# Kernel optimization log

Hardware: AMD Instinct MI355X
Metric: run time of the kernel (lower is better)

## Reference

```python
import jax, jax.numpy as jnp
import numpy as np

EMB = 64
HEADS = 8
B = 4
T = 2048


def setup_inputs() -> dict:
    key = jax.random.key(0)
    ks = jax.random.split(key, 7)
    s = 0.05
    x = jax.random.normal(ks[0], (B, T, EMB), dtype=jnp.float32)
    y = jax.random.normal(ks[1], (B, T, EMB), dtype=jnp.float32)
    mask = jax.random.randint(ks[2], (1, T, T), 0, 2, dtype=jnp.int32)
    Wk = jax.random.normal(ks[3], (EMB, EMB * HEADS), dtype=jnp.float32) * s
    Wq = jax.random.normal(ks[4], (EMB, EMB * HEADS), dtype=jnp.float32) * s
    Wv = jax.random.normal(ks[5], (EMB, EMB * HEADS), dtype=jnp.float32) * s
    Wu = jax.random.normal(ks[6], (EMB * HEADS, EMB), dtype=jnp.float32) * s
    bu = jnp.zeros((EMB,), dtype=jnp.float32)
    return {"x": x, "y": y, "mask": mask, "Wk": Wk, "Wq": Wq, "Wv": Wv, "Wu": Wu, "bu": bu}


def reference(x, y, mask, Wk, Wq, Wv, Wu, bu):
    b, t_x, e = x.shape
    _, t_y, _ = y.shape
    h = HEADS
    # projections: each head gets full dim e (head_dim == emb in this module)
    k = (x @ Wk).reshape(b, t_x, h, e).transpose(0, 2, 1, 3)  # [b,h,t_x,e]
    q = (y @ Wq).reshape(b, t_y, h, e).transpose(0, 2, 1, 3)  # [b,h,t_y,e]
    v = (x @ Wv).reshape(b, t_x, h, e).transpose(0, 2, 1, 3)  # [b,h,t_x,e]
    scale = jnp.asarray(e, x.dtype) ** 0.25
    q = q / scale
    k = k / scale
    dot = jnp.einsum('bhqe,bhke->bhqk', q, k)  # [b,h,t_y,t_x]
    # mask: [1,t_y,t_x] broadcast over batch*heads; fill -1e9 where mask==0
    dot = jnp.where(mask[:, None, :, :] == 0, jnp.asarray(-1e9, dot.dtype), dot)
    att = jax.nn.softmax(dot, axis=-1)
    out = jnp.einsum('bhqk,bhke->bqhe', att, v).reshape(b, t_y, h * e)
    return out @ Wu + bu
```

## Files before the change

### kernel.cpp

```cpp
#include <hip/hip_runtime.h>

#define EMB 64
#define HEADS 8
#define SEQ 2048
#define LSF 68

typedef short short8 __attribute__((ext_vector_type(8)));
typedef float f32x4 __attribute__((ext_vector_type(4)));
typedef unsigned int u32;

__device__ __forceinline__ float4 ld4(const float* p) { return *(const float4*)p; }
__device__ __forceinline__ float4 fmad4(float4 a, float s, float4 c) {
  c.x += a.x*s; c.y += a.y*s; c.z += a.z*s; c.w += a.w*s; return c;
}
__device__ __forceinline__ unsigned short f2bf(float f) {
  union { float f; unsigned u; } x; x.f = f;
  return (unsigned short)((x.u + 0x7fffu + ((x.u >> 16) & 1u)) >> 16);
}
__device__ __forceinline__ float bf2f(unsigned short s) {
  union { unsigned u; float f; } x; x.u = ((unsigned)s) << 16;
  return x.f;
}
__device__ __forceinline__ float bits2f(u32 u) {
  union { u32 u; float f; } x; x.u = u;
  return x.f;
}
__device__ __forceinline__ u32 cvtpk(float lo, float hi) {
  u32 r;
  asm("v_cvt_pk_bf16_f32 %0, %1, %2" : "=v"(r) : "v"(lo), "v"(hi));
  return r;
}
__device__ __forceinline__ float vexp2(float x) {
  float r;
  asm("v_exp_f32 %0, %1" : "=v"(r) : "v"(x));
  return r;
}
__device__ __forceinline__ void gload16(const void* g, void* l) {
  __builtin_amdgcn_global_load_lds((const __attribute__((address_space(1))) unsigned int*)g,
                                   (__attribute__((address_space(3))) unsigned int*)l, 16, 0, 0);
}

#define LOG2E 1.4426950408889634f
#define NC0  (-5.770780163555854f)

__global__ __launch_bounds__(256) void prep_kernel(
    const float* __restrict__ x, const float* __restrict__ y,
    const float* __restrict__ Wk, const float* __restrict__ Wq, const float* __restrict__ Wv,
    const int* __restrict__ mask, const float* __restrict__ Wu,
    unsigned short* __restrict__ Kbuf, unsigned short* __restrict__ Qbuf,
    unsigned short* __restrict__ VbufT, u32* __restrict__ pmask,
    unsigned short* __restrict__ WuThi, unsigned short* __restrict__ WuTlo)
{
  __shared__ float As[64][LSF];
  __shared__ float Bs[64][LSF];
  const int t = threadIdx.x;
  const int z = blockIdx.z;

  if (z == 3) {
    const int bid = blockIdx.x * 8 + blockIdx.y;
    #pragma unroll
    for (int it = 0; it < 8; ++it) {
      const int gid = bid * 2048 + it * 256 + t;
      const int i = gid & 7, ll = (gid >> 3) & 63, ww = (gid >> 9) & 3;
      const int kt = (gid >> 11) & 31, qblk = gid >> 16;
      const int qq = qblk*64 + ww*16 + (ll & 15);
      const int g = ll >> 4, c = i >> 1, rr = i & 1;
      const int kk = kt*64 + 16*c + 4*g + 2*rr;
      const int2 mm = *(const int2*)&mask[(size_t)qq * SEQ + kk];
      pmask[gid] = (mm.x ? 0xFFFFu : 0u) | (mm.y ? 0xFFFF0000u : 0u);
    }
    if (blockIdx.y == 7) {
      const int idx = blockIdx.x * 256 + t;
      const int k = idx >> 6, n = idx & 63;
      const float wv = Wu[(size_t)k * EMB + n];
      const unsigned short hi = f2bf(wv);
      const unsigned short lo = f2bf(wv - bf2f(hi));
      WuThi[(size_t)n * 512 + k] = hi;
      WuTlo[(size_t)n * 512 + k] = lo;
    }
    return;
  }

  const int rowblk = blockIdx.x;
  const int h = blockIdx.y;
  const float* __restrict__ in = (z == 2) ? y : x;
  const float* __restrict__ W = (z == 0) ? Wk : (z == 1) ? Wv : Wq;

  for (int i = t; i < 1024; i += 256) {
    const int r = i >> 4, c4 = (i & 15) << 2;
    *(float4*)&As[r][c4] = ld4(&in[(size_t)(rowblk*64 + r)*EMB + c4]);
    *(float4*)&Bs[r][c4] = ld4(&W[(size_t)r*(EMB*HEADS) + h*EMB + c4]);
  }
  __syncthreads();

  const int tr = (t >> 4) << 2;
  const int tc = (t & 15) << 2;
  float4 acc[4];
  #pragma unroll
  for (int i = 0; i < 4; ++i) acc[i] = (float4){0,0,0,0};
  #pragma unroll 8
  for (int k = 0; k < 64; ++k) {
    const float4 w = *(const float4*)&Bs[k][tc];
    #pragma unroll
    for (int i = 0; i < 4; ++i) acc[i] = fmad4(w, As[tr+i][k], acc[i]);
  }

  const int b = rowblk >> 5;
  const int tbase = (rowblk & 31) * 64;
  const int bh = b * HEADS + h;
  const float scale = (z == 2) ? 0.125f : 1.0f;

  if (z != 1) {
    unsigned short* __restrict__ dst = (z == 0) ? Kbuf : Qbuf;
    #pragma unroll
    for (int i = 0; i < 4; ++i) {
      ushort4 o;
      o.x = f2bf(acc[i].x * scale); o.y = f2bf(acc[i].y * scale);
      o.z = f2bf(acc[i].z * scale); o.w = f2bf(acc[i].w * scale);
      *(ushort4*)&dst[((size_t)bh*SEQ + tbase + tr + i)*EMB + tc] = o;
    }
  } else {
    __syncthreads();
    #pragma unroll
    for (int i = 0; i < 4; ++i) {
      As[tc+0][tr+i] = acc[i].x; As[tc+1][tr+i] = acc[i].y;
      As[tc+2][tr+i] = acc[i].z; As[tc+3][tr+i] = acc[i].w;
    }
    __syncthreads();
    #pragma unroll
    for (int i = 0; i < 4; ++i) {
      ushort4 o;
      o.x = f2bf(As[tr+i][tc+0]); o.y = f2bf(As[tr+i][tc+1]);
      o.z = f2bf(As[tr+i][tc+2]); o.w = f2bf(As[tr+i][tc+3]);
      *(ushort4*)&VbufT[((size_t)bh*EMB + tr + i)*SEQ + tbase + tc] = o;
    }
  }
}

__global__ __launch_bounds__(256, 4) void flash_kernel(
    const unsigned short* __restrict__ Qbuf, const unsigned short* __restrict__ Kbuf,
    const unsigned short* __restrict__ VbufT, const u32* __restrict__ Pmask,
    unsigned short* __restrict__ Oint)
{
  __shared__ alignas(16) char smem[40960];
  char* const K0 = smem;
  char* const K1 = smem + 8192;
  char* const V0 = smem + 16384;
  char* const V1 = smem + 24576;

  const int t = threadIdx.x;
  const int w = t >> 6, l = t & 63, g = l >> 4, q = l & 15;
  const int id = blockIdx.x;
  const int k_ = id >> 3;
  const int bh = (id & 7) * 4 + (k_ >> 5);
  const int qblk = k_ & 31;
  const int b = bh >> 3, h = bh & 7;

  short8 qf[2];
  {
    const unsigned short* qp = Qbuf + ((size_t)bh*SEQ + qblk*64 + w*16 + q)*EMB + g*8;
    qf[0] = *(const short8*)qp;
    qf[1] = *(const short8*)(qp + 32);
  }

  f32x4 oacc[4];
  #pragma unroll
  for (int c = 0; c < 4; ++c) oacc[c] = (f32x4){0.f,0.f,0.f,0.f};
  const f32x4 z4 = (f32x4){0.f,0.f,0.f,0.f};
  float lsum = 0.f;

  char* const Pw = smem + 32768 + w*2048;
  const int sw = (q & 7) << 4;

  const u32* mp = Pmask + ((size_t)(qblk*128 + w))*512 + l*8;

  const int unit0 = w*64 + l, unit1 = 256 + w*64 + l;
  const int row0 = unit0 >> 3, row1 = unit1 >> 3;
  const int gs0 = (unit0 & 7) ^ (row0 & 7), gs1 = (unit1 & 7) ^ (row1 & 7);
  const unsigned short* kp0 = Kbuf + ((size_t)bh*SEQ + row0)*EMB + gs0*8;
  const unsigned short* kp1 = Kbuf + ((size_t)bh*SEQ + row1)*EMB + gs1*8;
  const unsigned short* vp0 = VbufT + ((size_t)bh*EMB + row0)*SEQ + gs0*8;
  const unsigned short* vp1 = VbufT + ((size_t)bh*EMB + row1)*SEQ + gs1*8;

  #define STAGE(KDST, VDST) do {                                                      \
    gload16(kp0, (KDST) + (w*64)*16);                                                 \
    gload16(vp0, (VDST) + (w*64)*16);                                                 \
    gload16(kp1, (KDST) + (256 + w*64)*16);                                           \
    gload16(vp1, (VDST) + (256 + w*64)*16);                                           \
    kp0 += 64*EMB; kp1 += 64*EMB; vp0 += 64; vp1 += 64;                               \
  } while (0)

  STAGE(K0, V0);
  __syncthreads();

  uint4 mw0 = *(const uint4*)mp;
  uint4 mw1 = *(const uint4*)(mp + 4);
  mp += 2048;

  #define TILE(kbase, vbase, DOSTAGE, nkdst, nvdst) do {                               \
    f32x4 sacc[4];                                                                     \
    __builtin_amdgcn_s_setprio(1);                                                     \
    _Pragma("unroll") for (int c = 0; c < 4; ++c) {                                    \
      const short8 kf0 = *(const short8*)((kbase) + (16*c + q)*128 + ((g<<4) ^ sw));   \
      const short8 kf1 = *(const short8*)((kbase) + (16*c + q)*128 + (((4+g)<<4) ^ sw));\
      sacc[c] = __builtin_amdgcn_mfma_f32_16x16x32_bf16(kf0, qf[0], z4, 0,0,0);        \
      sacc[c] = __builtin_amdgcn_mfma_f32_16x16x32_bf16(kf1, qf[1], sacc[c], 0,0,0);   \
    }                                                                                  \
    __builtin_amdgcn_s_setprio(0);                                                     \
    if (DOSTAGE) { STAGE(nkdst, nvdst); }           \
    uint4 mn0 = mw0, mn1 = mw1;                                                        \
    if (DOSTAGE) { mn0 = *(const uint4*)mp; mn1 = *(const uint4*)(mp + 4); mp += 2048; } \
    u32 pw[8];                                                                         \
    _Pragma("unroll") for (int c = 0; c < 4; ++c) {                                    \
      const float p0 = vexp2(fmaf(sacc[c][0], LOG2E, NC0));                            \
      const float p1 = vexp2(fmaf(sacc[c][1], LOG2E, NC0));                            \
      const float p2 = vexp2(fmaf(sacc[c][2], LOG2E, NC0));                            \
      const float p3 = vexp2(fmaf(sacc[c][3], LOG2E, NC0));                            \
      pw[2*c]   = cvtpk(p0, p1);                                                       \
      pw[2*c+1] = cvtpk(p2, p3);                                                       \
    }                                                                                  \
    pw[0] &= mw0.x; pw[1] &= mw0.y; pw[2] &= mw0.z; pw[3] &= mw0.w;                    \
    pw[4] &= mw1.x; pw[5] &= mw1.y; pw[6] &= mw1.z; pw[7] &= mw1.w;                    \
    _Pragma("unroll") for (int c = 0; c < 4; ++c)                                      \
      *(uint2*)(Pw + ((q*128 + 32*c + 8*g) ^ sw)) = make_uint2(pw[2*c], pw[2*c+1]);    \
    float ts = 0.f;                                                                    \
    _Pragma("unroll") for (int i = 0; i < 8; ++i)                                      \
      ts += bits2f(pw[i] << 16) + bits2f(pw[i] & 0xFFFF0000u);                         \
    ts += __shfl_xor(ts, 16);                                                          \
    ts += __shfl_xor(ts, 32);                                                          \
    lsum += ts;                                                                        \
    __builtin_amdgcn_sched_barrier(0);     \
    short8 pf[2];                                                                      \
    pf[0] = *(const short8*)(Pw + ((q*128 + 16*g) ^ sw));                              \
    pf[1] = *(const short8*)(Pw + ((q*128 + 64 + 16*g) ^ sw));                         \
    __builtin_amdgcn_s_setprio(1);                                                     \
    _Pragma("unroll") for (int c = 0; c < 4; ++c) {                                    \
      const short8 vf0 = *(const short8*)((vbase) + (16*c + q)*128 + ((g<<4) ^ sw));   \
      const short8 vf1 = *(const short8*)((vbase) + (16*c + q)*128 + (((4+g)<<4) ^ sw));\
      oacc[c] = __builtin_amdgcn_mfma_f32_16x16x32_bf16(pf[0], vf0, oacc[c], 0,0,0);   \
      oacc[c] = __builtin_amdgcn_mfma_f32_16x16x32_bf16(pf[1], vf1, oacc[c], 0,0,0);   \
    }                                                                                  \
    __builtin_amdgcn_s_setprio(0);                                                     \
    mw0 = mn0; mw1 = mn1;                                                              \
    __syncthreads();     \
  } while (0)

  #pragma unroll 1
  for (int kt2 = 0; kt2 < 16; ++kt2) {
    TILE(K0, V0, true,       K1, V1);
    TILE(K1, V1, (kt2 < 15), K0, V0);
  }
  #undef TILE
  #undef STAGE

  #pragma unroll
  for (int r = 0; r < 4; ++r) {
    const float lr = __shfl(lsum, (l & 48) | (4*g + r));
    const float inv = (lr > 1e-30f) ? 1.f / lr : 0.f;
    #pragma unroll
    for (int c = 0; c < 4; ++c) {
      Oint[((size_t)b*SEQ + qblk*64 + w*16 + 4*g + r)*(EMB*HEADS) + h*EMB + q + 16*c] =
          f2bf(oacc[c][r] * inv);
    }
  }
}

__global__ __launch_bounds__(128) void outproj_kernel(
    const unsigned short* __restrict__ Oint, const unsigned short* __restrict__ WuThi,
    const unsigned short* __restrict__ WuTlo, const float* __restrict__ bu,
    float* __restrict__ out)
{
  const int t = threadIdx.x;
  const int w = t >> 6, l = t & 63, g = l >> 4, q15 = l & 15;
  const int t0 = (blockIdx.x * 2 + w) * 16;
  const f32x4 z4 = (f32x4){0.f,0.f,0.f,0.f};
  f32x4 acc[4] = {z4, z4, z4, z4};

  #pragma unroll 2
  for (int kt = 0; kt < 16; ++kt) {
    const short8 af = *(const short8*)&Oint[(size_t)(t0 + q15)*512 + kt*32 + g*8];
    #pragma unroll
    for (int nt = 0; nt < 4; ++nt) {
      const short8 bh_ = *(const short8*)&WuThi[(size_t)(nt*16 + q15)*512 + kt*32 + g*8];
      const short8 bl_ = *(const short8*)&WuTlo[(size_t)(nt*16 + q15)*512 + kt*32 + g*8];
      acc[nt] = __builtin_amdgcn_mfma_f32_16x16x32_bf16(af, bh_, acc[nt], 0,0,0);
      acc[nt] = __builtin_amdgcn_mfma_f32_16x16x32_bf16(af, bl_, acc[nt], 0,0,0);
    }
  }

  #pragma unroll
  for (int nt = 0; nt < 4; ++nt) {
    const float bv = bu[nt*16 + q15];
    #pragma unroll
    for (int r = 0; r < 4; ++r)
      out[(size_t)(t0 + 4*g + r)*EMB + nt*16 + q15] = acc[nt][r] + bv;
  }
}

extern "C" void kernel_launch(void* const* d_in, const int* in_sizes, int n_in,
                              void* d_out, int out_size, void* d_ws, size_t ws_size,
                              hipStream_t stream) {
  const float* x   = (const float*)d_in[0];
  const float* y   = (const float*)d_in[1];
  const int*   mask= (const int*)d_in[2];
  const float* Wk  = (const float*)d_in[3];
  const float* Wq  = (const float*)d_in[4];
  const float* Wv  = (const float*)d_in[5];
  const float* Wu  = (const float*)d_in[6];
  const float* bu  = (const float*)d_in[7];
  float* out = (float*)d_out;

  unsigned short* Qbuf  = (unsigned short*)d_ws;
  unsigned short* Kbuf  = Qbuf + (size_t)32*SEQ*EMB;
  unsigned short* VbufT = Kbuf + (size_t)32*SEQ*EMB;
  u32* Pmask = (u32*)((char*)d_ws + (size_t)24*1024*1024);
  unsigned short* Oint  = (unsigned short*)((char*)d_ws + (size_t)32*1024*1024);
  unsigned short* WuThi = (unsigned short*)((char*)d_ws + (size_t)40*1024*1024);
  unsigned short* WuTlo = WuThi + 32768;

  prep_kernel<<<dim3(128, 8, 4), 256, 0, stream>>>(x, y, Wk, Wq, Wv, mask, Wu,
                                                   Kbuf, Qbuf, VbufT, Pmask, WuThi, WuTlo);
  flash_kernel<<<1024, 256, 0, stream>>>(Qbuf, Kbuf, VbufT, Pmask, Oint);
  outproj_kernel<<<256, 128, 0, stream>>>(Oint, WuThi, WuTlo, bu, out);
}
```

Before: 98.91 us.

## Move QKV projections to bf16x3 MFMA with a pre-split hi/lo kernel

Replaces the FP32 LDS-tiled FMA projection GEMM in the prep kernel with bf16 MFMA instructions. A new split kernel first converts x, y and the Wk/Wv/Wq weights into bf16 hi/lo pairs, with the weights transposed, so the projection can use three MFMAs per tile and keep near-FP32 accuracy. This targets the scalar-FMA cost of the projections but adds one more kernel launch and extra global traffic for the split buffers. The outputs are now written as scalar 2-byte stores instead of vector stores, including strided transposed stores for V.

New measurement: 110.1 us. +11.3%, slower.

```diff
diff --git a/kernel.cpp b/kernel.cpp
--- a/kernel.cpp
+++ b/kernel.cpp
@@ -3,16 +3,13 @@
 #define EMB 64
 #define HEADS 8
 #define SEQ 2048
-#define LSF 68
 
 typedef short short8 __attribute__((ext_vector_type(8)));
 typedef float f32x4 __attribute__((ext_vector_type(4)));
 typedef unsigned int u32;
+typedef unsigned short ushort_t;
 
 __device__ __forceinline__ float4 ld4(const float* p) { return *(const float4*)p; }
-__device__ __forceinline__ float4 fmad4(float4 a, float s, float4 c) {
-  c.x += a.x*s; c.y += a.y*s; c.z += a.z*s; c.w += a.w*s; return c;
-}
 __device__ __forceinline__ unsigned short f2bf(float f) {
   union { float f; unsigned u; } x; x.f = f;
   return (unsigned short)((x.u + 0x7fffu + ((x.u >> 16) & 1u)) >> 16);
@@ -43,16 +40,49 @@
 #define LOG2E 1.4426950408889634f
 #define NC0  (-5.770780163555854f)
 
-__global__ __launch_bounds__(256) void prep_kernel(
+__global__ __launch_bounds__(256) void split_kernel(
     const float* __restrict__ x, const float* __restrict__ y,
     const float* __restrict__ Wk, const float* __restrict__ Wq, const float* __restrict__ Wv,
-    const int* __restrict__ mask, const float* __restrict__ Wu,
+    unsigned short* __restrict__ xhi, unsigned short* __restrict__ xlo,
+    unsigned short* __restrict__ yhi, unsigned short* __restrict__ ylo,
+    unsigned short* __restrict__ WT)
+{
+  const int gid = blockIdx.x * 256 + threadIdx.x;
+  if (blockIdx.x < 1024) {
+    const int i4 = gid & 131071;
+    const bool isY = gid >= 131072;
+    const float4 v = ld4((isY ? y : x) + (size_t)i4 * 4);
+    ushort4 hi, lo;
+    hi.x = f2bf(v.x); lo.x = f2bf(v.x - bf2f(hi.x));
+    hi.y = f2bf(v.y); lo.y = f2bf(v.y - bf2f(hi.y));
+    hi.z = f2bf(v.z); lo.z = f2bf(v.z - bf2f(hi.z));
+    hi.w = f2bf(v.w); lo.w = f2bf(v.w - bf2f(hi.w));
+    *(ushort4*)&(isY ? yhi : xhi)[(size_t)i4 * 4] = hi;
+    *(ushort4*)&(isY ? ylo : xlo)[(size_t)i4 * 4] = lo;
+  } else {
+    const int e = gid - 1024 * 256;
+    if (e >= 98304) return;
+    const int z = e >> 15;
+    const int nk = e & 32767;
+    const int n = nk >> 6, k = nk & 63;
+    const float* __restrict__ W = (z == 0) ? Wk : (z == 1) ? Wv : Wq;
+    const float wv = W[(size_t)k * (EMB * HEADS) + n];
+    const unsigned short hi = f2bf(wv);
+    const unsigned short lo = f2bf(wv - bf2f(hi));
+    WT[(size_t)z * 65536 + nk] = hi;
+    WT[(size_t)z * 65536 + 32768 + nk] = lo;
+  }
+}
+
+__global__ __launch_bounds__(256) void projmfma_kernel(
+    const unsigned short* __restrict__ xhi, const unsigned short* __restrict__ xlo,
+    const unsigned short* __restrict__ yhi, const unsigned short* __restrict__ ylo,
+    const unsigned short* __restrict__ WT, const int* __restrict__ mask,
+    const float* __restrict__ Wu,
     unsigned short* __restrict__ Kbuf, unsigned short* __restrict__ Qbuf,
     unsigned short* __restrict__ VbufT, u32* __restrict__ pmask,
     unsigned short* __restrict__ WuThi, unsigned short* __restrict__ WuTlo)
 {
-  __shared__ float As[64][LSF];
-  __shared__ float Bs[64][LSF];
   const int t = threadIdx.x;
   const int z = blockIdx.z;
 
@@ -81,59 +111,65 @@
     return;
   }
 
+  const int wv_ = t >> 6, l = t & 63, g = l >> 4, q15 = l & 15;
   const int rowblk = blockIdx.x;
   const int h = blockIdx.y;
-  const float* __restrict__ in = (z == 2) ? y : x;
-  const float* __restrict__ W = (z == 0) ? Wk : (z == 1) ? Wv : Wq;
-
-  for (int i = t; i < 1024; i += 256) {
-    const int r = i >> 4, c4 = (i & 15) << 2;
-    *(float4*)&As[r][c4] = ld4(&in[(size_t)(rowblk*64 + r)*EMB + c4]);
-    *(float4*)&Bs[r][c4] = ld4(&W[(size_t)r*(EMB*HEADS) + h*EMB + c4]);
-  }
-  __syncthreads();
-
-  const int tr = (t >> 4) << 2;
-  const int tc = (t & 15) << 2;
-  float4 acc[4];
+  const int b = rowblk >> 5, bh = b * HEADS + h;
+  const int trow0 = rowblk * 64 + wv_ * 16;
+  const int tloc0 = (rowblk & 31) * 64 + wv_ * 16;
+  const f32x4 z4 = (f32x4){0.f,0.f,0.f,0.f};
+
+  const unsigned short* __restrict__ Ahi = (z == 2) ? yhi : xhi;
+  const unsigned short* __restrict__ Alo = (z == 2) ? ylo : xlo;
+  const unsigned short* __restrict__ WTz = WT + (size_t)z * 65536;
+
+  short8 xh[2], xl[2];
   #pragma unroll
-  for (int i = 0; i < 4; ++i) acc[i] = (float4){0,0,0,0};
-  #pragma unroll 8
-  for (int k = 0; k < 64; ++k) {
-    const float4 w = *(const float4*)&Bs[k][tc];
-    #pragma unroll
-    for (int i = 0; i < 4; ++i) acc[i] = fmad4(w, As[tr+i][k], acc[i]);
-  }
-
-  const int b = rowblk >> 5;
-  const int tbase = (rowblk & 31) * 64;
-  const int bh = b * HEADS + h;
-  const float scale = (z == 2) ? 0.125f : 1.0f;
+  for (int kt = 0; kt < 2; ++kt) {
+    xh[kt] = *(const short8*)&Ahi[(size_t)(trow0 + q15)*64 + kt*32 + g*8];
+    xl[kt] = *(const short8*)&Alo[(size_t)(trow0 + q15)*64 + kt*32 + g*8];
+  }
 
   if (z != 1) {
+    f32x4 acc[4];
+    #pragma unroll
+    for (int nt = 0; nt < 4; ++nt) {
+      acc[nt] = z4;
+      #pragma unroll
+      for (int kt = 0; kt < 2; ++kt) {
+        const short8 bh_ = *(const short8*)&WTz[(size_t)(h*64 + nt*16 + q15)*64 + kt*32 + g*8];
+        const short8 bl_ = *(const short8*)&WTz[32768 + (size_t)(h*64 + nt*16 + q15)*64 + kt*32 + g*8];
+        acc[nt] = __builtin_amdgcn_mfma_f32_16x16x32_bf16(xh[kt], bh_, acc[nt], 0,0,0);
+        acc[nt] = __builtin_amdgcn_mfma_f32_16x16x32_bf16(xh[kt], bl_, acc[nt], 0,0,0);
+        acc[nt] = __builtin_amdgcn_mfma_f32_16x16x32_bf16(xl[kt], bh_, acc[nt], 0,0,0);
+      }
+    }
+    const float scale = (z == 2) ? 0.125f : 1.0f;
     unsigned short* __restrict__ dst = (z == 0) ? Kbuf : Qbuf;
     #pragma unroll
-    for (int i = 0; i < 4; ++i) {
-      ushort4 o;
-      o.x = f2bf(acc[i].x * scale); o.y = f2bf(acc[i].y * scale);
-      o.z = f2bf(acc[i].z * scale); o.w = f2bf(acc[i].w * scale);
-      *(ushort4*)&dst[((size_t)bh*SEQ + tbase + tr + i)*EMB + tc] = o;
-    }
+    for (int nt = 0; nt < 4; ++nt)
+      #pragma unroll
+      for (int r = 0; r < 4; ++r)
+        dst[((size_t)bh*SEQ + tloc0 + 4*g + r)*64 + nt*16 + q15] = f2bf(acc[nt][r] * scale);
   } else {
-    __syncthreads();
-    #pragma unroll
-    for (int i = 0; i < 4; ++i) {
-      As[tc+0][tr+i] = acc[i].x; As[tc+1][tr+i] = acc[i].y;
-      As[tc+2][tr+i] = acc[i].z; As[tc+3][tr+i] = acc[i].w;
-    }
-    __syncthreads();
-    #pragma unroll
-    for (int i = 0; i < 4; ++i) {
-      ushort4 o;
-      o.x = f2bf(As[tr+i][tc+0]); o.y = f2bf(As[tr+i][tc+1]);
-      o.z = f2bf(As[tr+i][tc+2]); o.w = f2bf(As[tr+i][tc+3]);
-      *(ushort4*)&VbufT[((size_t)bh*EMB + tr + i)*SEQ + tbase + tc] = o;
-    }
+    f32x4 acc[4];
+    #pragma unroll
+    for (int mt = 0; mt < 4; ++mt) {
+      acc[mt] = z4;
+      #pragma unroll
+      for (int kt = 0; kt < 2; ++kt) {
+        const short8 ah_ = *(const short8*)&WTz[(size_t)(h*64 + mt*16 + q15)*64 + kt*32 + g*8];
+        const short8 al_ = *(const short8*)&WTz[32768 + (size_t)(h*64 + mt*16 + q15)*64 + kt*32 + g*8];
+        acc[mt] = __builtin_amdgcn_mfma_f32_16x16x32_bf16(ah_, xh[kt], acc[mt], 0,0,0);
+        acc[mt] = __builtin_amdgcn_mfma_f32_16x16x32_bf16(al_, xh[kt], acc[mt], 0,0,0);
+        acc[mt] = __builtin_amdgcn_mfma_f32_16x16x32_bf16(ah_, xl[kt], acc[mt], 0,0,0);
+      }
+    }
+    #pragma unroll
+    for (int mt = 0; mt < 4; ++mt)
+      #pragma unroll
+      for (int r = 0; r < 4; ++r)
+        VbufT[((size_t)bh*EMB + mt*16 + 4*g + r)*SEQ + tloc0 + q15] = f2bf(acc[mt][r]);
   }
 }
 
@@ -317,9 +353,15 @@
   unsigned short* Oint  = (unsigned short*)((char*)d_ws + (size_t)32*1024*1024);
   unsigned short* WuThi = (unsigned short*)((char*)d_ws + (size_t)40*1024*1024);
   unsigned short* WuTlo = WuThi + 32768;
-
-  prep_kernel<<<dim3(128, 8, 4), 256, 0, stream>>>(x, y, Wk, Wq, Wv, mask, Wu,
-                                                   Kbuf, Qbuf, VbufT, Pmask, WuThi, WuTlo);
+  unsigned short* xhi = (unsigned short*)((char*)d_ws + (size_t)40*1024*1024 + 131072);
+  unsigned short* xlo = xhi + 524288;
+  unsigned short* yhi = xlo + 524288;
+  unsigned short* ylo = yhi + 524288;
+  unsigned short* WT  = ylo + 524288;
+
+  split_kernel<<<1408, 256, 0, stream>>>(x, y, Wk, Wq, Wv, xhi, xlo, yhi, ylo, WT);
+  projmfma_kernel<<<dim3(128, 8, 4), 256, 0, stream>>>(xhi, xlo, yhi, ylo, WT, mask, Wu,
+                                                       Kbuf, Qbuf, VbufT, Pmask, WuThi, WuTlo);
   flash_kernel<<<1024, 256, 0, stream>>>(Qbuf, Kbuf, VbufT, Pmask, Oint);
   outproj_kernel<<<256, 128, 0, stream>>>(Oint, WuThi, WuTlo, bu, out);
 }
```
